# Performance work log

Hardware: AMD Instinct MI355X
Metric: run time of the kernel (lower is better)

## Reference

```python
import jax, jax.numpy as jnp
import numpy as np

B, S, D, H = 2, 2048, 1024, 16
DH = D // H

def setup_inputs() -> dict:
    key = jax.random.key(0)
    ks = jax.random.split(key, 12)
    def lin(kw, kb, fan_in):
        bound = 1.0 / np.sqrt(fan_in)
        W = jax.random.uniform(kw, (D, D), jnp.float32, -bound, bound)
        b = jax.random.uniform(kb, (D,), jnp.float32, -bound, bound)
        return W, b
    Wq, bq = lin(ks[0], ks[1], D)
    Wk, bk = lin(ks[2], ks[3], D)
    Wv, bv = lin(ks[4], ks[5], D)
    Wo, bo = lin(ks[6], ks[7], D)
    q = jax.random.normal(ks[8], (B, S, D), jnp.float32)
    k = jax.random.normal(ks[9], (B, S, D), jnp.float32)
    v = jax.random.normal(ks[10], (B, S, D), jnp.float32)
    # causal mask (1 = keep, 0 = masked), broadcastable to [B,H,S,S]
    mask = jnp.tril(jnp.ones((S, S), jnp.int32))[None, None, :, :]
    return {"q": q, "k": k, "v": v, "mask": mask,
            "Wq": Wq, "bq": bq, "Wk": Wk, "bk": bk,
            "Wv": Wv, "bv": bv, "Wo": Wo, "bo": bo}

def reference(q, k, v, mask, Wq, bq, Wk, bk, Wv, bv, Wo, bo):
    # projections: torch Linear is x @ W.T + b
    def split(x):  # [B,S,D] -> [B,H,S,DH]
        return x.reshape(B, S, H, DH).transpose(0, 2, 1, 3)
    qh = split(q @ Wq.T + bq)
    kh = split(k @ Wk.T + bk)
    vh = split(v @ Wv.T + bv)
    score = jnp.einsum('bhqd,bhkd->bhqk', qh, kh) / jnp.sqrt(jnp.float32(DH))
    score = jnp.where(mask == 0, jnp.float32(-1e9), score)
    attn = jax.nn.softmax(score, axis=-1)
    out = jnp.einsum('bhqk,bhkd->bhqd', attn, vh)
    out = out.transpose(0, 2, 1, 3).reshape(B, S, D)
    return out @ Wo.T + bo, attn
```

## Files before the change

kernel.cpp:

```cpp
#include <hip/hip_runtime.h>

#define S_LEN 2048
#define D_MODEL 1024
#define N_HEADS 16
#define D_HEAD 64
#define BATCH 2

typedef __bf16 bf16;
typedef __bf16 bf16x8 __attribute__((ext_vector_type(8)));
typedef __bf16 bf16x4 __attribute__((ext_vector_type(4)));
typedef float f32x4 __attribute__((ext_vector_type(4)));

__device__ __forceinline__ f32x4 mfma16(bf16x8 a, bf16x8 b, f32x4 c) {
  return __builtin_amdgcn_mfma_f32_16x16x32_bf16(a, b, c, 0, 0, 0);
}

__device__ __forceinline__ void gload16(const bf16* g, bf16* lds) {
  __builtin_amdgcn_global_load_lds((const __attribute__((address_space(1))) void*)g,
                                   (__attribute__((address_space(3))) void*)lds, 16, 0, 0);
}

__global__ __launch_bounds__(256) void cvt_w(
    const float* __restrict__ s0, const float* __restrict__ s1,
    const float* __restrict__ s2, const float* __restrict__ s3,
    bf16* __restrict__ d0, bf16* __restrict__ d1, bf16* __restrict__ d2,
    bf16* __restrict__ d3) {
  const int y = blockIdx.y;
  const float* s = (y == 0) ? s0 : (y == 1) ? s1 : (y == 2) ? s2 : s3;
  bf16* d = (y == 0) ? d0 : (y == 1) ? d1 : (y == 2) ? d2 : d3;
  const int i = blockIdx.x * blockDim.x + threadIdx.x;
  const f32x4 a = *(const f32x4*)(s + (size_t)i * 8);
  const f32x4 b = *(const f32x4*)(s + (size_t)i * 8 + 4);
  bf16x8 o;
  o[0] = (bf16)a[0]; o[1] = (bf16)a[1]; o[2] = (bf16)a[2]; o[3] = (bf16)a[3];
  o[4] = (bf16)b[0]; o[5] = (bf16)b[1]; o[6] = (bf16)b[2]; o[7] = (bf16)b[3];
  *(bf16x8*)(d + (size_t)i * 8) = o;
}

__device__ __forceinline__ void gemm_loop(const bf16* __restrict__ gA,
                                          const bf16* __restrict__ gB,
                                          bf16* As, bf16* Bs,
                                          f32x4 (&acc)[4][4], int tid) {
  const int l = tid & 63;
  const int w = tid >> 6;
  const int wr = w >> 1, wc = w & 1;
  const int lr = l & 15, lg = l >> 4;
  const int lrow8 = l >> 3;
  const int colg = ((l & 7) ^ (lrow8 & 7)) * 8;

  for (int k0 = 0; k0 < D_MODEL; k0 += 64) {
#pragma unroll
    for (int i = 0; i < 4; ++i) {
      const int c = w * 4 + i;
      const int row = c * 8 + lrow8;
      gload16(gA + (size_t)row * D_MODEL + k0 + colg, As + c * 512);
      gload16(gB + (size_t)row * D_MODEL + k0 + colg, Bs + c * 512);
    }
    __syncthreads();
#pragma unroll
    for (int half = 0; half < 2; ++half) {
      bf16x8 af[4], bfb[4];
#pragma unroll
      for (int mm = 0; mm < 4; ++mm) {
        const int row = wr * 64 + mm * 16 + lr;
        af[mm] = *(const bf16x8*)(As + row * 64 + ((half * 4 + lg) ^ (lr & 7)) * 8);
      }
#pragma unroll
      for (int nn = 0; nn < 4; ++nn) {
        const int row = wc * 64 + nn * 16 + lr;
        bfb[nn] = *(const bf16x8*)(Bs + row * 64 + ((half * 4 + lg) ^ (lr & 7)) * 8);
      }
#pragma unroll
      for (int mm = 0; mm < 4; ++mm)
#pragma unroll
        for (int nn = 0; nn < 4; ++nn)
          acc[mm][nn] = mfma16(af[mm], bfb[nn], acc[mm][nn]);
    }
    __syncthreads();
  }
}

__device__ __forceinline__ void gemm_loop_af32(const float* __restrict__ gA32,
                                               const bf16* __restrict__ gB,
                                               bf16* As, bf16* Bs,
                                               f32x4 (&acc)[4][4], int tid) {
  const int l = tid & 63;
  const int w = tid >> 6;
  const int wr = w >> 1, wc = w & 1;
  const int lr = l & 15, lg = l >> 4;
  const int lrow8 = l >> 3;
  const int colg = ((l & 7) ^ (lrow8 & 7)) * 8;

  const int arow = tid >> 1;
  const int ahalf = tid & 1;
  const float* aptr = gA32 + (size_t)arow * D_MODEL + ahalf * 32;
  bf16* awr = As + arow * 64;

  for (int k0 = 0; k0 < D_MODEL; k0 += 64) {
    f32x4 av[8];
#pragma unroll
    for (int c = 0; c < 8; ++c) av[c] = *(const f32x4*)(aptr + k0 + c * 4);
#pragma unroll
    for (int i = 0; i < 4; ++i) {
      const int c = w * 4 + i;
      const int row = c * 8 + lrow8;
      gload16(gB + (size_t)row * D_MODEL + k0 + colg, Bs + c * 512);
    }
#pragma unroll
    for (int c8 = 0; c8 < 4; ++c8) {
      bf16x8 o;
#pragma unroll
      for (int e = 0; e < 4; ++e) {
        o[e] = (bf16)av[c8 * 2][e];
        o[e + 4] = (bf16)av[c8 * 2 + 1][e];
      }
      const int col16 = ahalf * 4 + c8;
      *(bf16x8*)(awr + (col16 ^ (arow & 7)) * 8) = o;
    }
    __syncthreads();
#pragma unroll
    for (int half = 0; half < 2; ++half) {
      bf16x8 af[4], bfb[4];
#pragma unroll
      for (int mm = 0; mm < 4; ++mm) {
        const int row = wr * 64 + mm * 16 + lr;
        af[mm] = *(const bf16x8*)(As + row * 64 + ((half * 4 + lg) ^ (lr & 7)) * 8);
      }
#pragma unroll
      for (int nn = 0; nn < 4; ++nn) {
        const int row = wc * 64 + nn * 16 + lr;
        bfb[nn] = *(const bf16x8*)(Bs + row * 64 + ((half * 4 + lg) ^ (lr & 7)) * 8);
      }
#pragma unroll
      for (int mm = 0; mm < 4; ++mm)
#pragma unroll
        for (int nn = 0; nn < 4; ++nn)
          acc[mm][nn] = mfma16(af[mm], bfb[nn], acc[mm][nn]);
    }
    __syncthreads();
  }
}

__global__ __launch_bounds__(256) void gemm_qkv(
    const float* __restrict__ qf, const float* __restrict__ kf,
    const float* __restrict__ vf, const bf16* __restrict__ Wqb,
    const bf16* __restrict__ Wkb, const bf16* __restrict__ Wvb,
    const float* __restrict__ biasq, const float* __restrict__ biask,
    const float* __restrict__ biasv, bf16* __restrict__ qhw,
    bf16* __restrict__ khw, bf16* __restrict__ vtw) {
  __shared__ bf16 As[128 * 64];
  __shared__ bf16 Bs[128 * 64];
  __shared__ bf16 T[128][72];
  const int z = blockIdx.z;
  const float* A = (z == 0) ? qf : (z == 1) ? kf : vf;
  const bf16* W = (z == 0) ? Wqb : (z == 1) ? Wkb : Wvb;
  const float* bias = (z == 0) ? biasq : (z == 1) ? biask : biasv;
  const float scale = (z == 0) ? 0.125f : 1.0f;
  bf16* out = (z == 0) ? qhw : (z == 1) ? khw : vtw;

  const int tid = threadIdx.x;
  const int l = tid & 63;
  const int w = tid >> 6;
  const int wr = w >> 1, wc = w & 1;
  const int lr = l & 15, lg = l >> 4;

  f32x4 acc[4][4] = {};
  gemm_loop_af32(A + ((size_t)blockIdx.x * 128) * D_MODEL,
                 W + ((size_t)blockIdx.y * 128) * D_MODEL, As, Bs, acc, tid);

  const int b = (blockIdx.x * 128) >> 11;
  const int s0 = (blockIdx.x * 128) & 2047;

  if (z == 2) {
#pragma unroll
    for (int half = 0; half < 2; ++half) {
      if (wc == half) {
#pragma unroll
        for (int nn = 0; nn < 4; ++nn) {
          const int n = blockIdx.y * 128 + half * 64 + nn * 16 + lr;
          const float bv = bias[n];
#pragma unroll
          for (int mm = 0; mm < 4; ++mm)
#pragma unroll
            for (int r = 0; r < 4; ++r) {
              const int ml = wr * 64 + mm * 16 + lg * 4 + r;
              T[ml][nn * 16 + lr] = (bf16)(acc[mm][nn][r] + bv);
            }
        }
      }
      __syncthreads();
      const int d = tid & 63;
      const int sblk = (tid >> 6) * 32;
      const int hglob = blockIdx.y * 2 + half;
      bf16* orow = vtw + (((size_t)(b * N_HEADS + hglob)) * D_HEAD + d) * S_LEN + s0 + sblk;
#pragma unroll
      for (int j = 0; j < 4; ++j) {
        bf16x8 pk;
#pragma unroll
        for (int e = 0; e < 8; ++e) pk[e] = T[sblk + j * 8 + e][d];
        *(bf16x8*)(orow + j * 8) = pk;
      }
      __syncthreads();
    }
  } else {
#pragma unroll
    for (int half = 0; half < 2; ++half) {
      if (wc == half) {
#pragma unroll
        for (int nn = 0; nn < 4; ++nn) {
          const int n = blockIdx.y * 128 + half * 64 + nn * 16 + lr;
          const float bv = bias[n];
#pragma unroll
          for (int mm = 0; mm < 4; ++mm)
#pragma unroll
            for (int r = 0; r < 4; ++r) {
              const int ml = wr * 64 + mm * 16 + lg * 4 + r;
              T[ml][nn * 16 + lr] = (bf16)((acc[mm][nn][r] + bv) * scale);
            }
        }
      }
      __syncthreads();
      const int hglob = blockIdx.y * 2 + half;
      bf16* obase = out + ((size_t)(b * N_HEADS + hglob) * S_LEN + s0) * D_HEAD;
      const int rsub = tid >> 3;
      const int d8 = (tid & 7) * 8;
#pragma unroll
      for (int j = 0; j < 4; ++j) {
        const int row_l = j * 32 + rsub;
        *(bf16x8*)(obase + (size_t)row_l * D_HEAD + d8) = *(const bf16x8*)(&T[row_l][d8]);
      }
      __syncthreads();
    }
  }
}

__device__ __forceinline__ void stage_strip(const bf16* __restrict__ src,
                                            size_t rstride, bf16* lds, int tid) {
#pragma unroll
  for (int rnd = 0; rnd < 2; ++rnd) {
    const int chunk = rnd * 256 + tid;
    const int row = chunk >> 3;
    const int c8 = chunk & 7;
    const int src8 = c8 ^ (row & 7);
    gload16(src + (size_t)row * rstride + src8 * 8, lds + chunk * 8);
  }
}

__global__ __launch_bounds__(256) void attn_flash(
    const bf16* __restrict__ qh, const bf16* __restrict__ kh,
    const bf16* __restrict__ vt, bf16* __restrict__ ctx,
    float* __restrict__ lbuf, float* __restrict__ attn) {
  __shared__ bf16 Kb[2][64 * 64];
  __shared__ bf16 Vb[2][64 * 64];
  __shared__ bf16 P[4][16][72];
  const int tid = threadIdx.x;
  const int w = tid >> 6, l = tid & 63;
  const int lr = l & 15, lg = l >> 4;
  const int bh = blockIdx.y;
  const int bxx = blockIdx.x;

  if (bxx >= 32) {
    int rem = bxx - 32, zq = 0, cnt = 7;
    while (rem >= cnt) { rem -= cnt; --cnt; ++zq; }
    const int kq = zq + 1 + rem;
    float* base = attn + (size_t)bh * S_LEN * S_LEN + (size_t)(zq * 256) * S_LEN + kq * 256;
    const f32x4 zv = {};
    for (int it = 0; it < 64; ++it) {
      float* rp = base + (size_t)(it * 4 + w) * S_LEN + l * 4;
      __builtin_nontemporal_store(zv, (f32x4*)rp);
    }
    return;
  }

  const int qgroup = (bxx & 1) ? (31 - (bxx >> 1)) : (bxx >> 1);
  const int q0 = qgroup * 64 + w * 16;
  const int qrow = q0 + lr;
  const bf16* qp = qh + (size_t)bh * S_LEN * D_HEAD;
  const bf16* kp = kh + (size_t)bh * S_LEN * D_HEAD;
  const bf16* vp = vt + (size_t)bh * D_HEAD * S_LEN;

  const bf16x8 qf0 = *(const bf16x8*)(qp + (size_t)qrow * D_HEAD + lg * 8);
  const bf16x8 qf1 = *(const bf16x8*)(qp + (size_t)qrow * D_HEAD + 32 + lg * 8);

  const float NINF = -__builtin_inff();
  const int nfull = qgroup;
  const int x0 = (lg ^ (lr & 7)) * 8;
  const int x1 = ((4 | lg) ^ (lr & 7)) * 8;

  stage_strip(kp, D_HEAD, Kb[0], tid);
  stage_strip(vp, S_LEN, Vb[0], tid);
  __syncthreads();

  float lsum = 0.f;
  f32x4 oacc[4] = {};
  int cur = 0;

  for (int st = 0; st < nfull; ++st) {
    stage_strip(kp + (size_t)(st + 1) * 64 * D_HEAD, D_HEAD, Kb[cur ^ 1], tid);
    stage_strip(vp + (st + 1) * 64, S_LEN, Vb[cur ^ 1], tid);

    float ps = 0.f;
    __builtin_amdgcn_s_setprio(1);
    f32x4 zz4[4];
#pragma unroll
    for (int t = 0; t < 4; ++t) {
      const bf16* krow = Kb[cur] + (t * 16 + lr) * 64;
      f32x4 zz = {};
      zz = mfma16(*(const bf16x8*)(krow + x0), qf0, zz);
      zz = mfma16(*(const bf16x8*)(krow + x1), qf1, zz);
      zz4[t] = zz;
    }
    __builtin_amdgcn_s_setprio(0);
#pragma unroll
    for (int t = 0; t < 4; ++t) {
      bf16x4 pk;
#pragma unroll
      for (int r = 0; r < 4; ++r) {
        const float e = __expf(fminf(zz4[t][r], 60.f));
        ps += e;
        pk[r] = (bf16)e;
      }
      *(bf16x4*)(&P[w][lr][t * 16 + lg * 4]) = pk;
    }
    ps += __shfl_xor(ps, 16);
    ps += __shfl_xor(ps, 32);
    lsum += ps;
    const bf16x8 pb0 = *(const bf16x8*)(&P[w][lr][lg * 8]);
    const bf16x8 pb1 = *(const bf16x8*)(&P[w][lr][32 + lg * 8]);
    __builtin_amdgcn_s_setprio(1);
#pragma unroll
    for (int dt = 0; dt < 4; ++dt) {
      const bf16* vrow = Vb[cur] + (dt * 16 + lr) * 64;
      oacc[dt] = mfma16(*(const bf16x8*)(vrow + x0), pb0, oacc[dt]);
      oacc[dt] = mfma16(*(const bf16x8*)(vrow + x1), pb1, oacc[dt]);
    }
    __builtin_amdgcn_s_setprio(0);
    __syncthreads();
    cur ^= 1;
  }

  {
    float ps = 0.f;
#pragma unroll
    for (int t = 0; t < 4; ++t) {
      bf16x4 pk;
      if (t <= w) {
        const bf16* krow = Kb[cur] + (t * 16 + lr) * 64;
        f32x4 zz = {};
        zz = mfma16(*(const bf16x8*)(krow + x0), qf0, zz);
        zz = mfma16(*(const bf16x8*)(krow + x1), qf1, zz);
#pragma unroll
        for (int r = 0; r < 4; ++r) {
          const float sv = (t == w && (lg * 4 + r) > lr) ? NINF : zz[r];
          const float e = __expf(fminf(sv, 60.f));
          ps += e;
          pk[r] = (bf16)e;
        }
      } else {
#pragma unroll
        for (int r = 0; r < 4; ++r) pk[r] = (bf16)0.f;
      }
      *(bf16x4*)(&P[w][lr][t * 16 + lg * 4]) = pk;
    }
    ps += __shfl_xor(ps, 16);
    ps += __shfl_xor(ps, 32);
    lsum += ps;
    const bf16x8 pb0 = *(const bf16x8*)(&P[w][lr][lg * 8]);
    const bf16x8 pb1 = *(const bf16x8*)(&P[w][lr][32 + lg * 8]);
#pragma unroll
    for (int dt = 0; dt < 4; ++dt) {
      const bf16* vrow = Vb[cur] + (dt * 16 + lr) * 64;
      oacc[dt] = mfma16(*(const bf16x8*)(vrow + x0), pb0, oacc[dt]);
      oacc[dt] = mfma16(*(const bf16x8*)(vrow + x1), pb1, oacc[dt]);
    }
  }

  const float invl = 1.0f / lsum;
  const int b = bh >> 4, h = bh & 15;
  bf16* crow = ctx + ((size_t)(b * S_LEN + qrow)) * D_MODEL + h * D_HEAD;
#pragma unroll
  for (int dt = 0; dt < 4; ++dt) {
    bf16x4 ov;
#pragma unroll
    for (int r = 0; r < 4; ++r) ov[r] = (bf16)(oacc[dt][r] * invl);
    *(bf16x4*)(crow + dt * 16 + lg * 4) = ov;
  }
  if (lg == 0) lbuf[(size_t)bh * S_LEN + qrow] = invl;
}

__global__ __launch_bounds__(256) void mat_out(
    const bf16* __restrict__ qh, const bf16* __restrict__ kh,
    const float* __restrict__ lbuf, float* __restrict__ attn,
    const bf16* __restrict__ ctxA, const bf16* __restrict__ Wo,
    const float* __restrict__ bo, float* __restrict__ outp) {
  __shared__ __align__(16) char smem[34048];
  const int bid = blockIdx.x;
  const int tid = threadIdx.x;
  const int w = tid >> 6, l = tid & 63;
  const int lr = l & 15, lg = l >> 4;

  if (bid < 256) {
    bf16* As = (bf16*)smem;
    bf16* Bs = (bf16*)(smem + 16384);
    const int bx = bid & 31, by = bid >> 5;
    const int wr = w >> 1, wc = w & 1;
    f32x4 acc[4][4] = {};
    gemm_loop(ctxA + ((size_t)bx * 128) * D_MODEL,
              Wo + ((size_t)by * 128) * D_MODEL, As, Bs, acc, tid);
    const int rowg0 = bx * 128 + wr * 64;
    const int colg0 = by * 128 + wc * 64;
#pragma unroll
    for (int nn = 0; nn < 4; ++nn) {
      const int n = colg0 + nn * 16 + lr;
      const float bv = bo[n];
#pragma unroll
      for (int mm = 0; mm < 4; ++mm)
#pragma unroll
        for (int r = 0; r < 4; ++r) {
          const int m = rowg0 + mm * 16 + lg * 4 + r;
          __builtin_nontemporal_store(acc[mm][nn][r] + bv,
                                      outp + (size_t)m * D_MODEL + n);
        }
    }
    return;
  }

  bf16* Pt = (bf16*)smem;
  const int mid = bid - 256;
  const int bh = mid / 144;
  int rem = mid - bh * 144;
  int g = 0;
  while (2 * (g + 1) * (g + 2) <= rem) ++g;
  const int rem2 = rem - 2 * g * (g + 1);
  const int q0t = 4 * g + rem2 / (g + 1);
  const int kq = rem2 - (g + 1) * (rem2 / (g + 1));
  const int q0 = q0t * 64;
  const int k0b = kq * 256;
  float* ap = attn + (size_t)bh * S_LEN * S_LEN;

  const int k0 = k0b + w * 64;
  if (k0 <= q0 + 63) {
    const bf16* qp = qh + (size_t)bh * S_LEN * D_HEAD;
    const bf16* kp = kh + (size_t)bh * S_LEN * D_HEAD;
    float iv[4];
#pragma unroll
    for (int qs = 0; qs < 4; ++qs)
      iv[qs] = lbuf[(size_t)bh * S_LEN + q0 + qs * 16 + lr];
    bf16x8 kf[4][2], qf[4][2];
#pragma unroll
    for (int kt = 0; kt < 4; ++kt) {
      kf[kt][0] = *(const bf16x8*)(kp + (size_t)(k0 + kt * 16 + lr) * D_HEAD + lg * 8);
      kf[kt][1] = *(const bf16x8*)(kp + (size_t)(k0 + kt * 16 + lr) * D_HEAD + 32 + lg * 8);
    }
#pragma unroll
    for (int qs = 0; qs < 4; ++qs) {
      qf[qs][0] = *(const bf16x8*)(qp + (size_t)(q0 + qs * 16 + lr) * D_HEAD + lg * 8);
      qf[qs][1] = *(const bf16x8*)(qp + (size_t)(q0 + qs * 16 + lr) * D_HEAD + 32 + lg * 8);
    }
    f32x4 acc[4][4] = {};
#pragma unroll
    for (int qs = 0; qs < 4; ++qs)
#pragma unroll
      for (int kt = 0; kt < 4; ++kt) {
        acc[qs][kt] = mfma16(kf[kt][0], qf[qs][0], acc[qs][kt]);
        acc[qs][kt] = mfma16(kf[kt][1], qf[qs][1], acc[qs][kt]);
      }
#pragma unroll
    for (int qs = 0; qs < 4; ++qs) {
      const int q = q0 + qs * 16 + lr;
#pragma unroll
      for (int kt = 0; kt < 4; ++kt) {
        const int kbase = k0 + kt * 16 + lg * 4;
        bf16x4 pk;
#pragma unroll
        for (int r = 0; r < 4; ++r) {
          const float pv = (kbase + r > q)
                               ? 0.f
                               : __expf(fminf(acc[qs][kt][r], 60.f)) * iv[qs];
          pk[r] = (bf16)pv;
        }
        *(bf16x4*)(Pt + (qs * 16 + lr) * 264 + w * 64 + kt * 16 + lg * 4) = pk;
      }
    }
  } else {
    const bf16x4 z4 = {};
#pragma unroll
    for (int j = 0; j < 16; ++j)
      *(bf16x4*)(Pt + (j * 4 + lg) * 264 + w * 64 + lr * 4) = z4;
  }
  __syncthreads();

#pragma unroll
  for (int j = 0; j < 4; ++j) {
    const int rowl = w * 16 + j * 4 + lg;
    float* rp = ap + (size_t)(q0 + rowl) * S_LEN + k0b + lr * 4;
#pragma unroll
    for (int sub = 0; sub < 4; ++sub) {
      const bf16x4 pk = *(const bf16x4*)(Pt + rowl * 264 + sub * 64 + lr * 4);
      f32x4 o;
      o[0] = (float)pk[0]; o[1] = (float)pk[1];
      o[2] = (float)pk[2]; o[3] = (float)pk[3];
      __builtin_nontemporal_store(o, (f32x4*)(rp + sub * 64));
    }
  }
}

extern "C" void kernel_launch(void* const* d_in, const int* in_sizes, int n_in,
                              void* d_out, int out_size, void* d_ws, size_t ws_size,
                              hipStream_t stream) {
  (void)in_sizes; (void)n_in; (void)out_size; (void)ws_size;
  const float* q  = (const float*)d_in[0];
  const float* k  = (const float*)d_in[1];
  const float* v  = (const float*)d_in[2];
  const float* Wq = (const float*)d_in[4];
  const float* bq = (const float*)d_in[5];
  const float* Wk = (const float*)d_in[6];
  const float* bk = (const float*)d_in[7];
  const float* Wv = (const float*)d_in[8];
  const float* bv = (const float*)d_in[9];
  const float* Wo = (const float*)d_in[10];
  const float* bo = (const float*)d_in[11];

  float* outp = (float*)d_out;
  float* attn = outp + (size_t)BATCH * S_LEN * D_MODEL;

  char* ws = (char*)d_ws;
  bf16* qhw  = (bf16*)(ws);
  bf16* khw  = (bf16*)(ws + (8u << 20));
  bf16* vtw  = (bf16*)(ws + (16u << 20));
  bf16* ctxb = (bf16*)(ws + (24u << 20));
  bf16* Wqb  = (bf16*)(ws + (32u << 20));
  bf16* Wkb  = (bf16*)(ws + (34u << 20));
  bf16* Wvb  = (bf16*)(ws + (36u << 20));
  bf16* Wob  = (bf16*)(ws + (38u << 20));
  float* lbuf = (float*)(ws + (40u << 20));

  dim3 bb(256);
  cvt_w<<<dim3(512, 4), bb, 0, stream>>>(Wq, Wk, Wv, Wo, Wqb, Wkb, Wvb, Wob);
  gemm_qkv<<<dim3(32, 8, 3), bb, 0, stream>>>(q, k, v, Wqb, Wkb, Wvb,
                                              bq, bk, bv, qhw, khw, vtw);
  attn_flash<<<dim3(60, 32), bb, 0, stream>>>(qhw, khw, vtw, ctxb, lbuf, attn);
  mat_out<<<dim3(256 + 4608), bb, 0, stream>>>(qhw, khw, lbuf, attn,
                                               ctxb, Wob, bo, outp);
}
```

Baseline: 266.4 us.

## Load K/V tiles directly from global memory into registers in flash attention

Removes the double-buffered LDS staging of K and V strips, which used async global-to-LDS loads and a block-wide barrier per step. Each wave now loads its K and V fragments straight from global memory into registers, and V loads are issued before the softmax so their latency can overlap it. This drops the per-iteration __syncthreads and frees LDS. In exchange, the four waves each re-read the same K/V from global or L2 with no cross-wave reuse, and nothing prefetches the next tile.

```diff
diff --git a/kernel.cpp b/kernel.cpp
--- a/kernel.cpp
+++ b/kernel.cpp
@@ -234,24 +234,10 @@
   }
 }
 
-__device__ __forceinline__ void stage_strip(const bf16* __restrict__ src,
-                                            size_t rstride, bf16* lds, int tid) {
-#pragma unroll
-  for (int rnd = 0; rnd < 2; ++rnd) {
-    const int chunk = rnd * 256 + tid;
-    const int row = chunk >> 3;
-    const int c8 = chunk & 7;
-    const int src8 = c8 ^ (row & 7);
-    gload16(src + (size_t)row * rstride + src8 * 8, lds + chunk * 8);
-  }
-}
-
 __global__ __launch_bounds__(256) void attn_flash(
     const bf16* __restrict__ qh, const bf16* __restrict__ kh,
     const bf16* __restrict__ vt, bf16* __restrict__ ctx,
     float* __restrict__ lbuf, float* __restrict__ attn) {
-  __shared__ bf16 Kb[2][64 * 64];
-  __shared__ bf16 Vb[2][64 * 64];
   __shared__ bf16 P[4][16][72];
   const int tid = threadIdx.x;
   const int w = tid >> 6, l = tid & 63;
@@ -284,33 +270,37 @@
 
   const float NINF = -__builtin_inff();
   const int nfull = qgroup;
-  const int x0 = (lg ^ (lr & 7)) * 8;
-  const int x1 = ((4 | lg) ^ (lr & 7)) * 8;
-
-  stage_strip(kp, D_HEAD, Kb[0], tid);
-  stage_strip(vp, S_LEN, Vb[0], tid);
-  __syncthreads();
 
   float lsum = 0.f;
   f32x4 oacc[4] = {};
-  int cur = 0;
 
   for (int st = 0; st < nfull; ++st) {
-    stage_strip(kp + (size_t)(st + 1) * 64 * D_HEAD, D_HEAD, Kb[cur ^ 1], tid);
-    stage_strip(vp + (st + 1) * 64, S_LEN, Vb[cur ^ 1], tid);
-
-    float ps = 0.f;
+    const size_t kst = (size_t)st * 64;
+    bf16x8 kk[8];
+#pragma unroll
+    for (int t = 0; t < 4; ++t) {
+      const bf16* krow = kp + (kst + t * 16 + lr) * D_HEAD;
+      kk[t * 2] = *(const bf16x8*)(krow + lg * 8);
+      kk[t * 2 + 1] = *(const bf16x8*)(krow + 32 + lg * 8);
+    }
     __builtin_amdgcn_s_setprio(1);
     f32x4 zz4[4];
 #pragma unroll
     for (int t = 0; t < 4; ++t) {
-      const bf16* krow = Kb[cur] + (t * 16 + lr) * 64;
       f32x4 zz = {};
-      zz = mfma16(*(const bf16x8*)(krow + x0), qf0, zz);
-      zz = mfma16(*(const bf16x8*)(krow + x1), qf1, zz);
+      zz = mfma16(kk[t * 2], qf0, zz);
+      zz = mfma16(kk[t * 2 + 1], qf1, zz);
       zz4[t] = zz;
     }
     __builtin_amdgcn_s_setprio(0);
+    bf16x8 vv[8];
+#pragma unroll
+    for (int dt = 0; dt < 4; ++dt) {
+      const bf16* vrow = vp + (size_t)(dt * 16 + lr) * S_LEN + kst;
+      vv[dt * 2] = *(const bf16x8*)(vrow + lg * 8);
+      vv[dt * 2 + 1] = *(const bf16x8*)(vrow + 32 + lg * 8);
+    }
+    float ps = 0.f;
 #pragma unroll
     for (int t = 0; t < 4; ++t) {
       bf16x4 pk;
@@ -330,25 +320,23 @@
     __builtin_amdgcn_s_setprio(1);
 #pragma unroll
     for (int dt = 0; dt < 4; ++dt) {
-      const bf16* vrow = Vb[cur] + (dt * 16 + lr) * 64;
-      oacc[dt] = mfma16(*(const bf16x8*)(vrow + x0), pb0, oacc[dt]);
-      oacc[dt] = mfma16(*(const bf16x8*)(vrow + x1), pb1, oacc[dt]);
+      oacc[dt] = mfma16(vv[dt * 2], pb0, oacc[dt]);
+      oacc[dt] = mfma16(vv[dt * 2 + 1], pb1, oacc[dt]);
     }
     __builtin_amdgcn_s_setprio(0);
-    __syncthreads();
-    cur ^= 1;
   }
 
   {
+    const size_t kst = (size_t)nfull * 64;
     float ps = 0.f;
 #pragma unroll
     for (int t = 0; t < 4; ++t) {
       bf16x4 pk;
       if (t <= w) {
-        const bf16* krow = Kb[cur] + (t * 16 + lr) * 64;
+        const bf16* krow = kp + (kst + t * 16 + lr) * D_HEAD;
         f32x4 zz = {};
-        zz = mfma16(*(const bf16x8*)(krow + x0), qf0, zz);
-        zz = mfma16(*(const bf16x8*)(krow + x1), qf1, zz);
+        zz = mfma16(*(const bf16x8*)(krow + lg * 8), qf0, zz);
+        zz = mfma16(*(const bf16x8*)(krow + 32 + lg * 8), qf1, zz);
 #pragma unroll
         for (int r = 0; r < 4; ++r) {
           const float sv = (t == w && (lg * 4 + r) > lr) ? NINF : zz[r];
@@ -369,9 +357,9 @@
     const bf16x8 pb1 = *(const bf16x8*)(&P[w][lr][32 + lg * 8]);
 #pragma unroll
     for (int dt = 0; dt < 4; ++dt) {
-      const bf16* vrow = Vb[cur] + (dt * 16 + lr) * 64;
-      oacc[dt] = mfma16(*(const bf16x8*)(vrow + x0), pb0, oacc[dt]);
-      oacc[dt] = mfma16(*(const bf16x8*)(vrow + x1), pb1, oacc[dt]);
+      const bf16* vrow = vp + (size_t)(dt * 16 + lr) * S_LEN + kst;
+      oacc[dt] = mfma16(*(const bf16x8*)(vrow + lg * 8), pb0, oacc[dt]);
+      oacc[dt] = mfma16(*(const bf16x8*)(vrow + 32 + lg * 8), pb1, oacc[dt]);
     }
   }
 
```

After: 434.3 us. +63.0%, slower.
